# Optimization experiments

Hardware: AMD Instinct MI355X
Metric: run time of the kernel (lower is better)

The kernel has to match this reference:

```python
import jax, jax.numpy as jnp
import numpy as np

BATCH, K_DIM, SEQ_L = 8, 1, 2048
D_MODEL, D_STATE, KCH = 256, 64, 2  # 64 complex states == d_state 128 real; 2 kernel channels (bidirectional)


def setup_inputs() -> dict:
    key = jax.random.key(0)
    ks = jax.random.split(key, 12)
    H, N = D_MODEL, D_STATE
    s = 1.0 / np.sqrt(H)
    # log-uniform timestep in [1e-3, 1e-1] as in S4 init
    dt = jnp.exp(jax.random.uniform(ks[2], (H,)) * (np.log(0.1) - np.log(0.001)) + np.log(0.001))
    return {
        "x": jax.random.normal(ks[0], (BATCH, H, K_DIM, SEQ_L), jnp.float32),
        "t": jax.random.normal(ks[1], (BATCH, 1, H), jnp.float32),
        "W_t": jax.random.normal(ks[3], (H, H)) * s,
        "b_t": jnp.zeros((H,)),
        "ln_g": jnp.ones((H,)),
        "ln_b": jnp.zeros((H,)),
        "log_dt": jnp.log(dt),
        "log_A_real": jnp.log(0.5 * jnp.ones((H, N))),
        "A_imag": jnp.tile(np.pi * jnp.arange(N, dtype=np.float32), (H, 1)),
        "B_re": jnp.ones((H, N)),
        "B_im": jnp.zeros((H, N)),
        "C_re": jax.random.normal(ks[4], (KCH, H, N)) * np.sqrt(0.5),
        "C_im": jax.random.normal(ks[5], (KCH, H, N)) * np.sqrt(0.5),
        "D": jax.random.normal(ks[6], (H,)),
        "W_out": jax.random.normal(ks[7], (H, H)) * s,
        "b_out": jnp.zeros((H,)),
        "W1": jax.random.normal(ks[8], (H, H)) * s,
        "b1": jnp.zeros((H,)),
        "W2": jax.random.normal(ks[9], (H, H)) * s,
        "b2": jnp.zeros((H,)),
    }


def _s4_kernel(log_dt, log_A_real, A_imag, B_re, B_im, C_re, C_im, L):
    # Diagonal SSM convolution kernel (ZOH discretization), 2 channels for bidirectional
    dt = jnp.exp(log_dt)[:, None]                      # (H,1)
    A = -jnp.exp(log_A_real) + 1j * A_imag             # (H,N)
    B = B_re + 1j * B_im                               # (H,N)
    C = C_re + 1j * C_im                               # (KCH,H,N)
    dtA = dt * A
    dB = B * (jnp.exp(dtA) - 1.0) / A                  # ZOH input discretization
    V = jnp.exp(dtA[:, :, None] * jnp.arange(L))       # (H,N,L) Vandermonde of dA^l
    return 2.0 * jnp.einsum('chn,hnl->chl', C * dB, V).real  # (KCH,H,L)


def _s4_layer(u, ln_g, ln_b, log_dt, log_A_real, A_imag, B_re, B_im, C_re, C_im, D, W_out, b_out):
    # u: (B*, H, L). Pre-LayerNorm over channels, S4 FFT conv, D skip, GELU, out proj, residual.
    mu = jnp.mean(u, axis=1, keepdims=True)
    var = jnp.var(u, axis=1, keepdims=True)
    z = (u - mu) / jnp.sqrt(var + 1e-5) * ln_g[:, None] + ln_b[:, None]
    L = u.shape[-1]
    k = _s4_kernel(log_dt, log_A_real, A_imag, B_re, B_im, C_re, C_im, L)
    # bidirectional: causal kernel + time-reversed kernel, combined at length 2L
    k_bi = jnp.pad(k[0], ((0, 0), (0, L))) + jnp.pad(k[1][:, ::-1], ((0, 0), (L, 0)))  # (H,2L)
    kf = jnp.fft.rfft(k_bi, n=2 * L)                   # (H,L+1)
    zf = jnp.fft.rfft(z, n=2 * L)                      # (B*,H,L+1)
    y = jnp.fft.irfft(zf * kf[None], n=2 * L)[..., :L]
    y = y + z * D[:, None]
    y = jax.nn.gelu(y, approximate=False)
    y = jnp.einsum('oh,bhl->bol', W_out, y) + b_out[:, None]  # transposed output linear
    return y + u


def reference(x, t, W_t, b_t, ln_g, ln_b, log_dt, log_A_real, A_imag, B_re, B_im, C_re, C_im, D, W_out, b_out, W1, b1, W2, b2):
    b, c, k, l = x.shape
    tt = jnp.einsum('boc,dc->bod', t, W_t) + b_t       # time_linear: (b,1,H)
    s4_in = x + tt[:, 0, :, None, None]                # 'b 1 c -> b c 1 1' broadcast
    u = s4_in.transpose(0, 2, 1, 3).reshape(b * k, c, l)  # 'b c k l -> (b k) c l'
    out = _s4_layer(u, ln_g, ln_b, log_dt, log_A_real, A_imag, B_re, B_im, C_re, C_im, D, W_out, b_out)
    out = out.reshape(b, k, c, l).transpose(0, 2, 1, 3)   # '(b k) c l -> b c k l'
    g = jnp.tanh(out) * jax.nn.sigmoid(out)            # WaveNet-style gate
    out1 = jnp.einsum('oc,bckl->bokl', W1, g) + b1[None, :, None, None]  # 1x1 conv2d
    out2 = jnp.einsum('oc,bckl->bokl', W2, g) + b2[None, :, None, None]
    return (out1 + x, out2)
```

## Files before the change

kernel.cpp:

```cpp
#include <hip/hip_runtime.h>
#include <math.h>

#define LL 2048
#define HH 256
#define BB 8
#define NN 64
#define HN (HH*NN)
#define ELEMS (BB*HH*LL)

typedef __attribute__((ext_vector_type(8))) short bf16x8v;
typedef __attribute__((ext_vector_type(4))) float f32x4v;

static inline __device__ ushort f2b_rne(float f) {
  uint u = __float_as_uint(f);
  return (ushort)((u + 0x7fffu + ((u >> 16) & 1u)) >> 16);
}
static inline __device__ float b2f(ushort u) { return __uint_as_float((uint)u << 16); }
#define UNPK(u, lo, hi) { lo = __uint_as_float((u)<<16); hi = __uint_as_float((u)&0xffff0000u); }

__global__ __launch_bounds__(256) void init_kernel(
    const float* __restrict__ t, const float* __restrict__ W_t, const float* __restrict__ b_t,
    const float* __restrict__ log_dt, const float* __restrict__ log_A_real,
    const float* __restrict__ A_imag,
    const float* __restrict__ B_re, const float* __restrict__ B_im,
    const float* __restrict__ C_re, const float* __restrict__ C_im,
    const float* __restrict__ Dp,
    const float* __restrict__ Wo, const float* __restrict__ W1, const float* __restrict__ W2,
    float* __restrict__ P, float* __restrict__ tt,
    ushort* __restrict__ Wob, ushort* __restrict__ W1b, ushort* __restrict__ W2b,
    ushort* __restrict__ Mc, ushort* __restrict__ Vc, ushort* __restrict__ Uc,
    float* __restrict__ rT) {
  int blk = blockIdx.x;
  int tid = threadIdx.x;
  if (blk < BB) {
    int b = blk, h = tid;
    float s = b_t[h];
    const float* trow = t + b*HH;
    const float* wrow = W_t + h*HH;
    for (int c = 0; c < HH; ++c) s = fmaf(trow[c], wrow[c], s);
    tt[b*HH + h] = s;
    return;
  }
  if (blk < BB + 192) {
    int q = blk - BB;
    int m = q >> 6;
    int i = (q & 63)*1024 + tid*4;
    const float* src = (m==0) ? Wo : (m==1 ? W1 : W2);
    ushort* dst = (m==0) ? Wob : (m==1 ? W1b : W2b);
    float4 v = *reinterpret_cast<const float4*>(src + i);
    union { ushort us[4]; uint2 u2; } pk;
    pk.us[0] = f2b_rne(v.x); pk.us[1] = f2b_rne(v.y);
    pk.us[2] = f2b_rne(v.z); pk.us[3] = f2b_rne(v.w);
    *reinterpret_cast<uint2*>(dst + i) = pk.u2;
    return;
  }
  int h = blk - (BB + 192);
  __shared__ float RRe[65][64], RIm[65][64];
  __shared__ float K0[64], K1[64];
  __shared__ float W0r[64], W0i[64], W1r[64], W1i[64];
  float dt = expf(log_dt[h]);
  for (int idx = tid; idx < 65*64; idx += 256) {
    int d = idx >> 6, n = idx & 63;
    float are = -expf(log_A_real[h*64+n]);
    float aim = A_imag[h*64+n];
    float ang = dt*aim*(float)d;
    float mag = expf(dt*are*(float)d);
    RRe[d][n] = mag * cosf(ang);
    RIm[d][n] = mag * sinf(ang);
  }
  __syncthreads();
  if (tid < 64) {
    int n = tid, gid = h*64 + n;
    float are = -expf(log_A_real[gid]);
    float aim = A_imag[gid];
    float rre = RRe[1][n], rim = RIm[1][n];
    float inv  = 1.0f / (are*are + aim*aim);
    float m_re = rre - 1.0f, m_im = rim;
    float q_re = (m_re*are + m_im*aim) * inv;
    float q_im = (m_im*are - m_re*aim) * inv;
    float bre = B_re[gid], bim = B_im[gid];
    float db_re = q_re*bre - q_im*bim;
    float db_im = q_re*bim + q_im*bre;
    float c0r = C_re[gid],      c0i = C_im[gid];
    float c1r = C_re[HN + gid], c1i = C_im[HN + gid];
    float w0r = 2.0f*(c0r*db_re - c0i*db_im), w0i = 2.0f*(c0r*db_im + c0i*db_re);
    float w1r = 2.0f*(c1r*db_re - c1i*db_im), w1i = 2.0f*(c1r*db_im + c1i*db_re);
    W0r[n] = w0r; W0i[n] = w0i; W1r[n] = w1r; W1i[n] = w1i;
    P[gid]        = w0r;
    P[HN + gid]   = w0i;
    P[2*HN + gid] = w1r;
    P[3*HN + gid] = w1i;
    rT[gid*2]   = RRe[64][n];
    rT[gid*2+1] = RIm[64][n];
  }
  __syncthreads();
  if (tid < 128) {
    int d = tid & 63; bool c1 = tid >= 64;
    float s = 0.f;
    if (!c1) for (int n = 0; n < 64; ++n) s += W0r[n]*RRe[d][n] - W0i[n]*RIm[d][n];
    else     for (int n = 0; n < 64; ++n) s += W1r[n]*RRe[d][n] - W1i[n]*RIm[d][n];
    if (c1) K1[d] = s; else K0[d] = s;
  }
  __syncthreads();
  float dh = Dp[h];
  for (int idx = tid; idx < 4096; idx += 256) {
    int i = idx >> 6, j = idx & 63;
    float v = (i > j) ? K0[i-j] : (i < j ? K1[j-i-1] : (K0[0] + dh));
    Mc[(size_t)h*4096 + idx] = f2b_rne(v);
  }
  for (int idx = tid; idx < 256*64; idx += 256) {
    int row = idx >> 6, j = idx & 63;
    int n = (row >> 1) & 63;
    bool im = row & 1, bwd = row >= 128;
    int d = bwd ? j : 63-j;
    Vc[(size_t)h*16384 + idx] = f2b_rne(im ? RIm[d][n] : RRe[d][n]);
  }
  for (int idx = tid; idx < 64*256; idx += 256) {
    int i = idx >> 8, col = idx & 255;
    int n = (col >> 1) & 63;
    bool im = col & 1, bwd = col >= 128;
    int d = bwd ? 63-i : i+1;
    Uc[(size_t)h*16384 + idx] = f2b_rne(im ? -RIm[d][n] : RRe[d][n]);
  }
}

__global__ __launch_bounds__(256) void lnz_kernel(
    const float* __restrict__ x, const float* __restrict__ tt,
    const float* __restrict__ ln_g, const float* __restrict__ ln_b,
    ushort* __restrict__ zb, ushort* __restrict__ xt) {
  int b  = blockIdx.x >> 6;
  int l0 = (blockIdx.x & 63) * 32;
  int tid = threadIdx.x;
  int r8 = tid >> 3;
  int c  = tid & 7;
  __shared__ ushort XS[256][36];
  __shared__ float SS[32][33], SS2[32][33];
  __shared__ float MU[32], RS[32];
  float s[4] = {0.f,0.f,0.f,0.f}, s2[4] = {0.f,0.f,0.f,0.f};
  #pragma unroll
  for (int it = 0; it < 8; ++it) {
    int h = it*32 + r8;
    float ttv = tt[b*HH + h];
    float vv[4];
    *reinterpret_cast<float4*>(vv) =
        *reinterpret_cast<const float4*>(x + (size_t)(b*HH + h)*LL + l0 + c*4);
    #pragma unroll
    for (int j = 0; j < 4; ++j) {
      float w = vv[j] + ttv;
      s[j] += w; s2[j] = fmaf(w, w, s2[j]);
      XS[h][c*4 + j] = f2b_rne(w);
    }
  }
  #pragma unroll
  for (int j = 0; j < 4; ++j) { SS[c*4+j][r8] = s[j]; SS2[c*4+j][r8] = s2[j]; }
  __syncthreads();
  if (tid < 32) {
    float a = 0.f, a2 = 0.f;
    #pragma unroll
    for (int p = 0; p < 32; ++p) { a += SS[tid][p]; a2 += SS2[tid][p]; }
    float m = a * (1.0f/HH);
    float var = a2 * (1.0f/HH) - m*m;
    MU[tid] = m;
    RS[tid] = 1.0f / sqrtf(var + 1e-5f);
  }
  __syncthreads();
  #pragma unroll
  for (int it = 0; it < 8; ++it) {
    int h = it*32 + r8;
    float gg = ln_g[h], bb2 = ln_b[h];
    uint2 u2 = *reinterpret_cast<const uint2*>(&XS[h][c*4]);
    float v0, v1, v2, v3;
    UNPK(u2.x, v0, v1); UNPK(u2.y, v2, v3);
    int l = c*4;
    float z0 = (v0 - MU[l])   * RS[l]   * gg + bb2;
    float z1 = (v1 - MU[l+1]) * RS[l+1] * gg + bb2;
    float z2 = (v2 - MU[l+2]) * RS[l+2] * gg + bb2;
    float z3 = (v3 - MU[l+3]) * RS[l+3] * gg + bb2;
    uint2 zo;
    zo.x = (uint)f2b_rne(z0) | ((uint)f2b_rne(z1) << 16);
    zo.y = (uint)f2b_rne(z2) | ((uint)f2b_rne(z3) << 16);
    size_t off = (size_t)(b*HH + h)*LL + l0 + l;
    *reinterpret_cast<uint2*>(zb + off) = zo;
    *reinterpret_cast<uint2*>(xt + off) = u2;
  }
}

__global__ __launch_bounds__(512) void ssm_all(
    const ushort* __restrict__ zb, const ushort* __restrict__ Vc,
    const ushort* __restrict__ Mc, const ushort* __restrict__ Uc,
    const float* __restrict__ P, const float* __restrict__ rT,
    ushort* __restrict__ g) {
  int h = blockIdx.x;
  int tid = threadIdx.x, wid = tid >> 6, lane = tid & 63;
  int row16 = lane & 15, kg = lane >> 4;
  __shared__ ushort G[256][260];

  #pragma unroll
  for (int rep = 0; rep < 2; ++rep) {
    int tile = wid + rep*8;
    int comp0 = (tile >> 2)*64, bct = (tile & 3)*64;
    f32x4v acc[4][4];
    #pragma unroll
    for (int fm = 0; fm < 4; ++fm)
      #pragma unroll
      for (int fn = 0; fn < 4; ++fn) acc[fm][fn] = (f32x4v){0.f,0.f,0.f,0.f};
    #pragma unroll
    for (int k0 = 0; k0 < 64; k0 += 32) {
      bf16x8v a[4], bv[4];
      #pragma unroll
      for (int fm = 0; fm < 4; ++fm)
        a[fm] = *reinterpret_cast<const bf16x8v*>(
            Vc + (size_t)h*16384 + (comp0 + fm*16 + row16)*64 + k0 + kg*8);
      #pragma unroll
      for (int fn = 0; fn < 4; ++fn) {
        int bc = bct + fn*16 + row16; int b = bc >> 5, c = bc & 31;
        bv[fn] = *reinterpret_cast<const bf16x8v*>(
            zb + ((size_t)(b*HH + h))*LL + c*64 + k0 + kg*8);
      }
      #pragma unroll
      for (int fm = 0; fm < 4; ++fm)
        #pragma unroll
        for (int fn = 0; fn < 4; ++fn)
          acc[fm][fn] = __builtin_amdgcn_mfma_f32_16x16x32_bf16(a[fm], bv[fn], acc[fm][fn], 0,0,0);
    }
    #pragma unroll
    for (int fm = 0; fm < 4; ++fm)
      #pragma unroll
      for (int fn = 0; fn < 4; ++fn) {
        int bc = bct + fn*16 + row16;
        int comp = comp0 + fm*16 + kg*4;
        union { ushort us[4]; uint2 u2; } pk;
        #pragma unroll
        for (int r = 0; r < 4; ++r) pk.us[r] = f2b_rne(acc[fm][fn][r]);
        *reinterpret_cast<uint2*>(&G[bc][comp]) = pk.u2;
      }
  }
  __syncthreads();

  #pragma unroll
  for (int rep = 0; rep < 2; ++rep) {
    int unit = wid + rep*8;
    int b = unit & 7, dir = unit >> 3;
    int n = lane;
    float w_re = dir ? P[2*HN + h*64+n] : P[h*64+n];
    float w_im = dir ? P[3*HN + h*64+n] : P[HN + h*64+n];
    float rtr = rT[(h*64+n)*2], rti = rT[(h*64+n)*2+1];
    float sre = 0.f, sim = 0.f;
    if (dir == 0) {
      for (int c = 0; c < 32; ++c) {
        uint* slot = reinterpret_cast<uint*>(&G[b*32 + c][2*n]);
        uint gg = *slot;
        float ure = w_re*sre - w_im*sim;
        float uim = w_re*sim + w_im*sre;
        *slot = (uint)f2b_rne(ure) | ((uint)f2b_rne(uim) << 16);
        float gre, gim; UNPK(gg, gre, gim);
        float nre = rtr*sre - rti*sim + gre;
        float nim = rtr*sim + rti*sre + gim;
        sre = nre; sim = nim;
      }
    } else {
      for (int c = 31; c >= 0; --c) {
        uint* slot = reinterpret_cast<uint*>(&G[b*32 + c][128 + 2*n]);
        uint gg = *slot;
        float ure = w_re*sre - w_im*sim;
        float uim = w_re*sim + w_im*sre;
        *slot = (uint)f2b_rne(ure) | ((uint)f2b_rne(uim) << 16);
        float gre, gim; UNPK(gg, gre, gim);
        float nre = rtr*sre - rti*sim + gre;
        float nim = rtr*sim + rti*sre + gim;
        sre = nre; sim = nim;
      }
    }
  }
  __syncthreads();

  {
    int i0 = (wid & 1)*32, bct = (wid >> 1)*64;
    f32x4v acc[2][4];
    #pragma unroll
    for (int fm = 0; fm < 2; ++fm)
      #pragma unroll
      for (int fn = 0; fn < 4; ++fn) acc[fm][fn] = (f32x4v){0.f,0.f,0.f,0.f};
    #pragma unroll
    for (int k0 = 0; k0 < 64; k0 += 32) {
      bf16x8v a[2], bv[4];
      #pragma unroll
      for (int fm = 0; fm < 2; ++fm)
        a[fm] = *reinterpret_cast<const bf16x8v*>(
            Mc + (size_t)h*4096 + (i0 + fm*16 + row16)*64 + k0 + kg*8);
      #pragma unroll
      for (int fn = 0; fn < 4; ++fn) {
        int bc = bct + fn*16 + row16; int b = bc >> 5, c = bc & 31;
        bv[fn] = *reinterpret_cast<const bf16x8v*>(
            zb + ((size_t)(b*HH + h))*LL + c*64 + k0 + kg*8);
      }
      #pragma unroll
      for (int fm = 0; fm < 2; ++fm)
        #pragma unroll
        for (int fn = 0; fn < 4; ++fn)
          acc[fm][fn] = __builtin_amdgcn_mfma_f32_16x16x32_bf16(a[fm], bv[fn], acc[fm][fn], 0,0,0);
    }
    #pragma unroll
    for (int k0 = 0; k0 < 256; k0 += 32) {
      bf16x8v a[2], bv[4];
      #pragma unroll
      for (int fm = 0; fm < 2; ++fm)
        a[fm] = *reinterpret_cast<const bf16x8v*>(
            Uc + (size_t)h*16384 + (i0 + fm*16 + row16)*256 + k0 + kg*8);
      #pragma unroll
      for (int fn = 0; fn < 4; ++fn)
        bv[fn] = *reinterpret_cast<const bf16x8v*>(&G[bct + fn*16 + row16][k0 + kg*8]);
      #pragma unroll
      for (int fm = 0; fm < 2; ++fm)
        #pragma unroll
        for (int fn = 0; fn < 4; ++fn)
          acc[fm][fn] = __builtin_amdgcn_mfma_f32_16x16x32_bf16(a[fm], bv[fn], acc[fm][fn], 0,0,0);
    }
    #pragma unroll
    for (int fm = 0; fm < 2; ++fm)
      #pragma unroll
      for (int fn = 0; fn < 4; ++fn) {
        int bc = bct + fn*16 + row16; int b = bc >> 5, c = bc & 31;
        int i = i0 + fm*16 + kg*4;
        union { ushort us[4]; uint2 u2; } pk;
        #pragma unroll
        for (int r = 0; r < 4; ++r) {
          float v = acc[fm][fn][r];
          float ge = 0.5f * v * (1.0f + erff(v * 0.70710678118654752f));
          pk.us[r] = f2b_rne(ge);
        }
        *reinterpret_cast<uint2*>(&g[((size_t)(b*HH + h))*LL + c*64 + i]) = pk.u2;
      }
  }
}

__global__ __launch_bounds__(256, 2) void fused_out(
    const ushort* __restrict__ g, const ushort* __restrict__ Wob,
    const ushort* __restrict__ W1b, const ushort* __restrict__ W2b,
    const float* __restrict__ b_out, const float* __restrict__ b1v,
    const float* __restrict__ b2v, const ushort* __restrict__ xt,
    const float* __restrict__ tt,
    float* __restrict__ out1, float* __restrict__ out2) {
  int l0 = blockIdx.x * 32;
  int b  = blockIdx.y;
  int tid = threadIdx.x, wid = tid >> 6, lane = tid & 63;
  int row16 = lane & 15, kg = lane >> 4;
  int o0 = wid * 64;

  __shared__ ushort Tg[32][274];
  __shared__ ushort X[256][38];

  bf16x8v wA[8][4];
  #pragma unroll
  for (int k8 = 0; k8 < 8; ++k8)
    #pragma unroll
    for (int fo = 0; fo < 4; ++fo)
      wA[k8][fo] = *reinterpret_cast<const bf16x8v*>(
          Wob + (size_t)(o0 + fo*16 + row16)*HH + k8*32 + kg*8);

  {
    const ushort* gsrc = g + (size_t)b*HH*LL + l0;
    int cq = tid & 7;
    #pragma unroll
    for (int p = 0; p < 8; ++p) {
      int h = p*32 + (tid >> 3);
      uint2 v = *reinterpret_cast<const uint2*>(gsrc + (size_t)h*LL + cq*4);
      union { uint2 u2; ushort us[4]; } pk; pk.u2 = v;
      #pragma unroll
      for (int j = 0; j < 4; ++j) Tg[cq*4 + j][h] = pk.us[j];
    }
  }
  {
    const ushort* xsrc = xt + (size_t)b*HH*LL + l0;
    int cq = tid & 7;
    #pragma unroll
    for (int p = 0; p < 8; ++p) {
      int o = p*32 + (tid >> 3);
      uint2 v = *reinterpret_cast<const uint2*>(xsrc + (size_t)o*LL + cq*4);
      *reinterpret_cast<uint2*>(&X[o][cq*4]) = v;
    }
  }
  float biasA[4][4];
  #pragma unroll
  for (int fo = 0; fo < 4; ++fo)
    #pragma unroll
    for (int r = 0; r < 4; ++r)
      biasA[fo][r] = b_out[o0 + fo*16 + kg*4 + r];
  __syncthreads();

  f32x4v accA[4][2];
  #pragma unroll
  for (int fo = 0; fo < 4; ++fo)
    #pragma unroll
    for (int fl = 0; fl < 2; ++fl) accA[fo][fl] = (f32x4v){0.f,0.f,0.f,0.f};
  #pragma unroll
  for (int k8 = 0; k8 < 8; ++k8) {
    bf16x8v bb[2];
    #pragma unroll
    for (int fl = 0; fl < 2; ++fl)
      bb[fl] = *reinterpret_cast<const bf16x8v*>(&Tg[fl*16+row16][k8*32 + kg*8]);
    #pragma unroll
    for (int fo = 0; fo < 4; ++fo)
      #pragma unroll
      for (int fl = 0; fl < 2; ++fl)
        accA[fo][fl] = __builtin_amdgcn_mfma_f32_16x16x32_bf16(wA[k8][fo], bb[fl], accA[fo][fl], 0,0,0);
  }
  bf16x8v w1[8][4];
  #pragma unroll
  for (int k8 = 0; k8 < 8; ++k8)
    #pragma unroll
    for (int fo = 0; fo < 4; ++fo)
      w1[k8][fo] = *reinterpret_cast<const bf16x8v*>(
          W1b + (size_t)(o0 + fo*16 + row16)*HH + k8*32 + kg*8);
  uint2 gw[4][2];
  #pragma unroll
  for (int fo = 0; fo < 4; ++fo)
    #pragma unroll
    for (int fl = 0; fl < 2; ++fl) {
      union { ushort us[4]; uint2 u2; } pk;
      #pragma unroll
      for (int r = 0; r < 4; ++r) {
        int o = o0 + fo*16 + kg*4 + r;
        int l = fl*16 + row16;
        float v = accA[fo][fl][r] + biasA[fo][r] + b2f(X[o][l]);
        float gate = tanhf(v) * (1.0f/(1.0f + expf(-v)));
        pk.us[r] = f2b_rne(gate);
      }
      gw[fo][fl] = pk.u2;
    }
  __syncthreads();
  #pragma unroll
  for (int fo = 0; fo < 4; ++fo)
    #pragma unroll
    for (int fl = 0; fl < 2; ++fl)
      *reinterpret_cast<uint2*>(&Tg[fl*16+row16][o0 + fo*16 + kg*4]) = gw[fo][fl];
  __syncthreads();

  {
    f32x4v p[2][4];
    #pragma unroll
    for (int fl = 0; fl < 2; ++fl)
      #pragma unroll
      for (int fo = 0; fo < 4; ++fo) p[fl][fo] = (f32x4v){0.f,0.f,0.f,0.f};
    #pragma unroll
    for (int k8 = 0; k8 < 8; ++k8) {
      bf16x8v bb[2];
      #pragma unroll
      for (int fl = 0; fl < 2; ++fl)
        bb[fl] = *reinterpret_cast<const bf16x8v*>(&Tg[fl*16+row16][k8*32 + kg*8]);
      #pragma unroll
      for (int fl = 0; fl < 2; ++fl)
        #pragma unroll
        for (int fo = 0; fo < 4; ++fo)
          p[fl][fo] = __builtin_amdgcn_mfma_f32_16x16x32_bf16(bb[fl], w1[k8][fo], p[fl][fo], 0,0,0);
    }
    #pragma unroll
    for (int k8 = 0; k8 < 8; ++k8)
      #pragma unroll
      for (int fo = 0; fo < 4; ++fo)
        wA[k8][fo] = *reinterpret_cast<const bf16x8v*>(
            W2b + (size_t)(o0 + fo*16 + row16)*HH + k8*32 + kg*8);
    #pragma unroll
    for (int fl = 0; fl < 2; ++fl)
      #pragma unroll
      for (int fo = 0; fo < 4; ++fo) {
        int o  = o0 + fo*16 + row16;
        int lb = fl*16 + kg*4;
        float bias = b1v[o] - tt[b*HH + o];
        uint2 xv = *reinterpret_cast<const uint2*>(&X[o][lb]);
        float x0, x1, x2, x3;
        UNPK(xv.x, x0, x1); UNPK(xv.y, x2, x3);
        float4 v;
        v.x = p[fl][fo][0] + bias + x0;
        v.y = p[fl][fo][1] + bias + x1;
        v.z = p[fl][fo][2] + bias + x2;
        v.w = p[fl][fo][3] + bias + x3;
        *reinterpret_cast<float4*>(&out1[((size_t)(b*HH + o))*LL + l0 + lb]) = v;
      }
  }
  {
    f32x4v q[2][4];
    #pragma unroll
    for (int fl = 0; fl < 2; ++fl)
      #pragma unroll
      for (int fo = 0; fo < 4; ++fo) q[fl][fo] = (f32x4v){0.f,0.f,0.f,0.f};
    #pragma unroll
    for (int k8 = 0; k8 < 8; ++k8) {
      bf16x8v bb[2];
      #pragma unroll
      for (int fl = 0; fl < 2; ++fl)
        bb[fl] = *reinterpret_cast<const bf16x8v*>(&Tg[fl*16+row16][k8*32 + kg*8]);
      #pragma unroll
      for (int fl = 0; fl < 2; ++fl)
        #pragma unroll
        for (int fo = 0; fo < 4; ++fo)
          q[fl][fo] = __builtin_amdgcn_mfma_f32_16x16x32_bf16(bb[fl], wA[k8][fo], q[fl][fo], 0,0,0);
    }
    #pragma unroll
    for (int fl = 0; fl < 2; ++fl)
      #pragma unroll
      for (int fo = 0; fo < 4; ++fo) {
        int o  = o0 + fo*16 + row16;
        int lb = fl*16 + kg*4;
        float bias = b2v[o];
        float4 v;
        v.x = q[fl][fo][0] + bias;
        v.y = q[fl][fo][1] + bias;
        v.z = q[fl][fo][2] + bias;
        v.w = q[fl][fo][3] + bias;
        *reinterpret_cast<float4*>(&out2[((size_t)(b*HH + o))*LL + l0 + lb]) = v;
      }
  }
}

extern "C" void kernel_launch(void* const* d_in, const int* in_sizes, int n_in,
                              void* d_out, int out_size, void* d_ws, size_t ws_size,
                              hipStream_t stream) {
  const float* x    = (const float*)d_in[0];
  const float* t    = (const float*)d_in[1];
  const float* W_t  = (const float*)d_in[2];
  const float* b_t  = (const float*)d_in[3];
  const float* ln_g = (const float*)d_in[4];
  const float* ln_b = (const float*)d_in[5];
  const float* log_dt = (const float*)d_in[6];
  const float* log_A_real = (const float*)d_in[7];
  const float* A_imag = (const float*)d_in[8];
  const float* B_re = (const float*)d_in[9];
  const float* B_im = (const float*)d_in[10];
  const float* C_re = (const float*)d_in[11];
  const float* C_im = (const float*)d_in[12];
  const float* Dp   = (const float*)d_in[13];
  const float* W_out= (const float*)d_in[14];
  const float* b_out= (const float*)d_in[15];
  const float* W1   = (const float*)d_in[16];
  const float* b1   = (const float*)d_in[17];
  const float* W2   = (const float*)d_in[18];
  const float* b2   = (const float*)d_in[19];

  float* out1 = (float*)d_out;
  float* out2 = out1 + ELEMS;

  float* P    = (float*)d_ws;
  float* tt   = P + 4*HN;
  float* rT   = tt + BB*HH;
  ushort* zb  = (ushort*)(rT + 2*HN);
  ushort* Mc  = zb + ELEMS;
  ushort* Vc  = Mc + (size_t)4096*HH;
  ushort* Uc  = Vc + (size_t)16384*HH;
  ushort* g   = Uc + (size_t)16384*HH;
  ushort* Wob = g + ELEMS;
  ushort* W1b = Wob + HH*HH;
  ushort* W2b = W1b + HH*HH;
  ushort* xt  = W2b + HH*HH;

  init_kernel<<<BB + 192 + HH, 256, 0, stream>>>(
      t, W_t, b_t, log_dt, log_A_real, A_imag, B_re, B_im, C_re, C_im, Dp,
      W_out, W1, W2, P, tt, Wob, W1b, W2b, Mc, Vc, Uc, rT);
  lnz_kernel<<<BB*64, 256, 0, stream>>>(x, tt, ln_g, ln_b, zb, xt);
  ssm_all<<<HH, 512, 0, stream>>>(zb, Vc, Mc, Uc, P, rT, g);
  fused_out<<<dim3(LL/32, BB), 256, 0, stream>>>(g, Wob, W1b, W2b, b_out, b1, b2,
                                                 xt, tt, out1, out2);
}
```

Before: 105.7 us.

## Split SSM chunk kernel across batch halves to double grid size

The ssm_all kernel now launches a 2x256 grid where each block handles 4 batches of one channel instead of all 8. Shared memory per block is halved, and each wave does one tile per phase instead of two; the scan phase uses all 8 waves once. The aim is to fill more of the MI355X's compute units with 512 blocks instead of 256, and to let more blocks fit per CU. The cost is that the V, M and U matrix loads are repeated in two blocks per channel.

```diff
diff --git a/kernel.cpp b/kernel.cpp
--- a/kernel.cpp
+++ b/kernel.cpp
@@ -190,15 +190,14 @@
     const ushort* __restrict__ Mc, const ushort* __restrict__ Uc,
     const float* __restrict__ P, const float* __restrict__ rT,
     ushort* __restrict__ g) {
-  int h = blockIdx.x;
+  int b0 = blockIdx.x * 4;
+  int h  = blockIdx.y;
   int tid = threadIdx.x, wid = tid >> 6, lane = tid & 63;
   int row16 = lane & 15, kg = lane >> 4;
-  __shared__ ushort G[256][260];
-
-  #pragma unroll
-  for (int rep = 0; rep < 2; ++rep) {
-    int tile = wid + rep*8;
-    int comp0 = (tile >> 2)*64, bct = (tile & 3)*64;
+  __shared__ ushort G[128][260];
+
+  {
+    int comp0 = (wid >> 1)*64, bct = (wid & 1)*64;
     f32x4v acc[4][4];
     #pragma unroll
     for (int fm = 0; fm < 4; ++fm)
@@ -213,7 +212,7 @@
             Vc + (size_t)h*16384 + (comp0 + fm*16 + row16)*64 + k0 + kg*8);
       #pragma unroll
       for (int fn = 0; fn < 4; ++fn) {
-        int bc = bct + fn*16 + row16; int b = bc >> 5, c = bc & 31;
+        int bc = bct + fn*16 + row16; int b = b0 + (bc >> 5), c = bc & 31;
         bv[fn] = *reinterpret_cast<const bf16x8v*>(
             zb + ((size_t)(b*HH + h))*LL + c*64 + k0 + kg*8);
       }
@@ -237,10 +236,8 @@
   }
   __syncthreads();
 
-  #pragma unroll
-  for (int rep = 0; rep < 2; ++rep) {
-    int unit = wid + rep*8;
-    int b = unit & 7, dir = unit >> 3;
+  {
+    int bloc = wid & 3, dir = wid >> 2;
     int n = lane;
     float w_re = dir ? P[2*HN + h*64+n] : P[h*64+n];
     float w_im = dir ? P[3*HN + h*64+n] : P[HN + h*64+n];
@@ -248,7 +245,7 @@
     float sre = 0.f, sim = 0.f;
     if (dir == 0) {
       for (int c = 0; c < 32; ++c) {
-        uint* slot = reinterpret_cast<uint*>(&G[b*32 + c][2*n]);
+        uint* slot = reinterpret_cast<uint*>(&G[bloc*32 + c][2*n]);
         uint gg = *slot;
         float ure = w_re*sre - w_im*sim;
         float uim = w_re*sim + w_im*sre;
@@ -260,7 +257,7 @@
       }
     } else {
       for (int c = 31; c >= 0; --c) {
-        uint* slot = reinterpret_cast<uint*>(&G[b*32 + c][128 + 2*n]);
+        uint* slot = reinterpret_cast<uint*>(&G[bloc*32 + c][128 + 2*n]);
         uint gg = *slot;
         float ure = w_re*sre - w_im*sim;
         float uim = w_re*sim + w_im*sre;
@@ -275,62 +272,44 @@
   __syncthreads();
 
   {
-    int i0 = (wid & 1)*32, bct = (wid >> 1)*64;
-    f32x4v acc[2][4];
-    #pragma unroll
-    for (int fm = 0; fm < 2; ++fm)
-      #pragma unroll
-      for (int fn = 0; fn < 4; ++fn) acc[fm][fn] = (f32x4v){0.f,0.f,0.f,0.f};
+    int i0 = (wid & 3)*16, bct = (wid >> 2)*64;
+    f32x4v acc[4];
+    #pragma unroll
+    for (int fn = 0; fn < 4; ++fn) acc[fn] = (f32x4v){0.f,0.f,0.f,0.f};
     #pragma unroll
     for (int k0 = 0; k0 < 64; k0 += 32) {
-      bf16x8v a[2], bv[4];
-      #pragma unroll
-      for (int fm = 0; fm < 2; ++fm)
-        a[fm] = *reinterpret_cast<const bf16x8v*>(
-            Mc + (size_t)h*4096 + (i0 + fm*16 + row16)*64 + k0 + kg*8);
+      bf16x8v a = *reinterpret_cast<const bf16x8v*>(
+          Mc + (size_t)h*4096 + (i0 + row16)*64 + k0 + kg*8);
       #pragma unroll
       for (int fn = 0; fn < 4; ++fn) {
-        int bc = bct + fn*16 + row16; int b = bc >> 5, c = bc & 31;
-        bv[fn] = *reinterpret_cast<const bf16x8v*>(
+        int bc = bct + fn*16 + row16; int b = b0 + (bc >> 5), c = bc & 31;
+        bf16x8v bv = *reinterpret_cast<const bf16x8v*>(
             zb + ((size_t)(b*HH + h))*LL + c*64 + k0 + kg*8);
-      }
-      #pragma unroll
-      for (int fm = 0; fm < 2; ++fm)
-        #pragma unroll
-        for (int fn = 0; fn < 4; ++fn)
-          acc[fm][fn] = __builtin_amdgcn_mfma_f32_16x16x32_bf16(a[fm], bv[fn], acc[fm][fn], 0,0,0);
+        acc[fn] = __builtin_amdgcn_mfma_f32_16x16x32_bf16(a, bv, acc[fn], 0,0,0);
+      }
     }
     #pragma unroll
     for (int k0 = 0; k0 < 256; k0 += 32) {
-      bf16x8v a[2], bv[4];
-      #pragma unroll
-      for (int fm = 0; fm < 2; ++fm)
-        a[fm] = *reinterpret_cast<const bf16x8v*>(
-            Uc + (size_t)h*16384 + (i0 + fm*16 + row16)*256 + k0 + kg*8);
-      #pragma unroll
-      for (int fn = 0; fn < 4; ++fn)
-        bv[fn] = *reinterpret_cast<const bf16x8v*>(&G[bct + fn*16 + row16][k0 + kg*8]);
-      #pragma unroll
-      for (int fm = 0; fm < 2; ++fm)
-        #pragma unroll
-        for (int fn = 0; fn < 4; ++fn)
-          acc[fm][fn] = __builtin_amdgcn_mfma_f32_16x16x32_bf16(a[fm], bv[fn], acc[fm][fn], 0,0,0);
-    }
-    #pragma unroll
-    for (int fm = 0; fm < 2; ++fm)
+      bf16x8v a = *reinterpret_cast<const bf16x8v*>(
+          Uc + (size_t)h*16384 + (i0 + row16)*256 + k0 + kg*8);
       #pragma unroll
       for (int fn = 0; fn < 4; ++fn) {
-        int bc = bct + fn*16 + row16; int b = bc >> 5, c = bc & 31;
-        int i = i0 + fm*16 + kg*4;
-        union { ushort us[4]; uint2 u2; } pk;
-        #pragma unroll
-        for (int r = 0; r < 4; ++r) {
-          float v = acc[fm][fn][r];
-          float ge = 0.5f * v * (1.0f + erff(v * 0.70710678118654752f));
-          pk.us[r] = f2b_rne(ge);
-        }
-        *reinterpret_cast<uint2*>(&g[((size_t)(b*HH + h))*LL + c*64 + i]) = pk.u2;
-      }
+        bf16x8v bv = *reinterpret_cast<const bf16x8v*>(&G[bct + fn*16 + row16][k0 + kg*8]);
+        acc[fn] = __builtin_amdgcn_mfma_f32_16x16x32_bf16(a, bv, acc[fn], 0,0,0);
+      }
+    }
+    #pragma unroll
+    for (int fn = 0; fn < 4; ++fn) {
+      int bc = bct + fn*16 + row16; int b = b0 + (bc >> 5), c = bc & 31;
+      union { ushort us[4]; uint2 u2; } pk;
+      #pragma unroll
+      for (int r = 0; r < 4; ++r) {
+        float v = acc[fn][r];
+        float ge = 0.5f * v * (1.0f + erff(v * 0.70710678118654752f));
+        pk.us[r] = f2b_rne(ge);
+      }
+      *reinterpret_cast<uint2*>(&g[((size_t)(b*HH + h))*LL + c*64 + i0 + kg*4]) = pk.u2;
+    }
   }
 }
 
@@ -557,7 +536,7 @@
       t, W_t, b_t, log_dt, log_A_real, A_imag, B_re, B_im, C_re, C_im, Dp,
       W_out, W1, W2, P, tt, Wob, W1b, W2b, Mc, Vc, Uc, rT);
   lnz_kernel<<<BB*64, 256, 0, stream>>>(x, tt, ln_g, ln_b, zb, xt);
-  ssm_all<<<HH, 512, 0, stream>>>(zb, Vc, Mc, Uc, P, rT, g);
+  ssm_all<<<dim3(2, HH), 512, 0, stream>>>(zb, Vc, Mc, Uc, P, rT, g);
   fused_out<<<dim3(LL/32, BB), 256, 0, stream>>>(g, Wob, W1b, W2b, b_out, b1, b2,
                                                  xt, tt, out1, out2);
 }
```

Measured after the change: 102.3 us. 1.03x faster.
